# Performance work log

Hardware: AMD Instinct MI355X
Metric: run time of the kernel (lower is better)

## Reference

```python
import jax, jax.numpy as jnp
import numpy as np

DEPTH = 4  # truncation depth of the tensor algebra


def _tprod(a, b):
    # tensor (outer) product of level-i and level-j terms, flattened row-major
    # a: (B, C^i), b: (B, C^j) -> (B, C^(i+j))
    return (a[:, :, None] * b[:, None, :]).reshape(a.shape[0], -1)


def _exp_levels(dx):
    # exp(dx) in the truncated tensor algebra: level k = dx^{\otimes k} / k!
    levels = [dx]
    for k in range(2, DEPTH + 1):
        levels.append(_tprod(levels[-1], dx) / k)
    return tuple(levels)


def _chen(a, b):
    # Chen's identity: (a \otimes b)_k = a_k + b_k + sum_{i=1}^{k-1} a_i \otimes b_{k-i}
    out = []
    for k in range(1, DEPTH + 1):
        t = a[k - 1] + b[k - 1]
        for i in range(1, k):
            t = t + _tprod(a[i - 1], b[k - 1 - i])
        out.append(t)
    return tuple(out)


def _log_levels(s):
    # log(1 + x) = sum_{n>=1} (-1)^{n+1}/n x^{\otimes n}, x = S - 1 (levels 1..DEPTH)
    res = list(s)
    power = [t for t in s]  # x^{\otimes 1}; entries may become None (structurally zero)
    for n in range(2, DEPTH + 1):
        new = [None] * DEPTH
        for k in range(n, DEPTH + 1):
            acc = None
            for i in range(n - 1, k):
                if power[i - 1] is None:
                    continue
                term = _tprod(power[i - 1], s[k - i - 1])
                acc = term if acc is None else acc + term
            new[k - 1] = acc
        power = new
        coef = ((-1.0) ** (n + 1)) / n
        for k in range(n, DEPTH + 1):
            if power[k - 1] is not None:
                res[k - 1] = res[k - 1] + coef * power[k - 1]
    return tuple(res)


def _logsignature(path):
    # path: (B, L, C); no basepoint, stream=False, inverse=False, mode='expand'
    dxs = jnp.moveaxis(path[:, 1:] - path[:, :-1], 1, 0)  # (L-1, B, C)
    init = _exp_levels(dxs[0])

    def step(carry, dx):
        return _chen(carry, _exp_levels(dx)), None

    sig, _ = jax.lax.scan(step, init, dxs[1:])
    logsig = _log_levels(sig)
    return jnp.concatenate(logsig, axis=-1)  # (B, C + C^2 + ... + C^DEPTH)


def setup_inputs() -> dict:
    key = jax.random.key(0)
    # scale so high tensor-algebra levels stay well-conditioned in fp32
    path = 0.1 * jax.random.normal(key, (64, 256, 16), dtype=jnp.float32)
    return {"path": path}


def reference(path):
    return _logsignature(path)
```

## Files before the change

### kernel.cpp

```cpp
#include <hip/hip_runtime.h>


#define NC 16
#define NL 256
#define NB 64
#define NSTEP 255
#define OUTB 69904
#define SIG123 4368
#define OFF_L2 16
#define OFF_L3 272
#define OFF_L4 4368

__global__ void k_dx(const float* __restrict__ path, float* __restrict__ dx) {
    int idx = blockIdx.x * blockDim.x + threadIdx.x;
    const int total = NB * NSTEP * NC;
    if (idx >= total) return;
    int i = idx & (NC - 1);
    int t = (idx >> 4) % NSTEP;
    int j = idx / (NC * NSTEP);
    dx[idx] = path[((size_t)j * NL + t + 1) * NC + i] - path[((size_t)j * NL + t) * NC + i];
}

__global__ __launch_bounds__(256, 4) void k_scan(const float* __restrict__ dx,
                                                 float* __restrict__ out,
                                                 float* __restrict__ sig123) {
    const int bid = blockIdx.x;
    const int j = bid >> 4;
    const int a = bid & 15;
    const int tid = threadIdx.x;
    const int b = tid >> 4;
    const int c = tid & 15;

    float s4[16];
#pragma unroll
    for (int d = 0; d < 16; ++d) s4[d] = 0.f;
    float s3 = 0.f, s2ab = 0.f, s1a = 0.f;

    const float* dxj = dx + (size_t)j * NSTEP * NC;

    for (int t = 0; t < NSTEP; ++t) {
        const float* r = dxj + t * NC;
        const float4 q0 = *(const float4*)(r);
        const float4 q1 = *(const float4*)(r + 4);
        const float4 q2 = *(const float4*)(r + 8);
        const float4 q3 = *(const float4*)(r + 12);
        const float dxa = r[a];
        const float dxb = r[b];
        const float dxc = r[c];

        const float pre4 = fmaf(dxb, fmaf(1.f / 6.f, s1a, (1.f / 24.f) * dxa), 0.5f * s2ab);
        const float T = fmaf(dxc, pre4, s3);

        const float dv[16] = {q0.x, q0.y, q0.z, q0.w, q1.x, q1.y, q1.z, q1.w,
                              q2.x, q2.y, q2.z, q2.w, q3.x, q3.y, q3.z, q3.w};
#pragma unroll
        for (int d = 0; d < 16; ++d) s4[d] = fmaf(dv[d], T, s4[d]);

        const float U = fmaf(dxb, fmaf(0.5f, s1a, (1.f / 6.f) * dxa), s2ab);
        s3 = fmaf(dxc, U, s3);
        s2ab = fmaf(dxb, fmaf(0.5f, dxa, s1a), s2ab);
        s1a += dxa;
    }

    float* outj = out + (size_t)j * OUTB;
    float* o4 = outj + OFF_L4 + ((a * 16 + b) * 16 + c) * 16;
#pragma unroll
    for (int d = 0; d < 16; d += 4)
        *(float4*)(o4 + d) = make_float4(s4[d], s4[d + 1], s4[d + 2], s4[d + 3]);

    float* sg = sig123 + (size_t)j * SIG123;
    sg[OFF_L3 + (a * 16 + b) * 16 + c] = s3;
    if (c == 0) sg[OFF_L2 + a * 16 + b] = s2ab;
    if (tid == 0) sg[a] = s1a;
}

__global__ __launch_bounds__(256) void k_log(const float* __restrict__ sig123,
                                             float* __restrict__ out) {
    const int bid = blockIdx.x;
    const int j = bid >> 4;
    const int a = bid & 15;
    const int tid = threadIdx.x;
    const int b = tid >> 4;
    const int c = tid & 15;

    const float* sg = sig123 + (size_t)j * SIG123;
    const float* s1 = sg;
    const float* s2 = sg + OFF_L2;
    const float* s3 = sg + OFF_L3;

    const float s1a = s1[a], s1b = s1[b], s1c = s1[c];
    const float s2ab = s2[a * 16 + b];
    const float s2bc = s2[b * 16 + c];
    const float s3abc = s3[(a * 16 + b) * 16 + c];

    float* outj = out + (size_t)j * OUTB;

    const float A = -0.5f * s1a;
    const float Bv = fmaf((1.f / 3.f) * s1a, s1b, -0.5f * s2ab);
    const float Cv = -0.5f * s3abc + (1.f / 3.f) * fmaf(s1a, s2bc, s2ab * s1c)
                     - 0.25f * s1a * s1b * s1c;

    float* o4 = outj + OFF_L4 + ((a * 16 + b) * 16 + c) * 16;
    const float* s3v = s3 + (b * 16 + c) * 16;
    const float* s2v = s2 + c * 16;
#pragma unroll
    for (int d0 = 0; d0 < 16; d0 += 4) {
        float4 v4 = *(const float4*)(o4 + d0);
        float4 v3 = *(const float4*)(s3v + d0);
        float4 v2 = *(const float4*)(s2v + d0);
        float4 v1 = *(const float4*)(s1 + d0);
        float4 rr;
        rr.x = fmaf(A, v3.x, v4.x) + fmaf(Bv, v2.x, Cv * v1.x);
        rr.y = fmaf(A, v3.y, v4.y) + fmaf(Bv, v2.y, Cv * v1.y);
        rr.z = fmaf(A, v3.z, v4.z) + fmaf(Bv, v2.z, Cv * v1.z);
        rr.w = fmaf(A, v3.w, v4.w) + fmaf(Bv, v2.w, Cv * v1.w);
        *(float4*)(o4 + d0) = rr;
    }

    const float r3 = s3abc - 0.5f * fmaf(s1a, s2bc, s2ab * s1c)
                     + (1.f / 3.f) * s1a * s1b * s1c;
    outj[OFF_L3 + (a * 16 + b) * 16 + c] = r3;
    if (c == 0) outj[OFF_L2 + a * 16 + b] = fmaf(-0.5f * s1a, s1b, s2ab);
    if (tid == 0) outj[a] = s1a;
}

extern "C" void kernel_launch(void* const* d_in, const int* in_sizes, int n_in,
                              void* d_out, int out_size, void* d_ws, size_t ws_size,
                              hipStream_t stream) {
    const float* path = (const float*)d_in[0];
    float* out = (float*)d_out;
    float* dx = (float*)d_ws;
    float* sig123 = dx + (size_t)NB * NSTEP * NC;

    const int total_dx = NB * NSTEP * NC;
    k_dx<<<(total_dx + 255) / 256, 256, 0, stream>>>(path, dx);
    k_scan<<<NB * 16, 256, 0, stream>>>(dx, out, sig123);
    k_log<<<NB * 16, 256, 0, stream>>>(sig123, out);
}
```

Before: 130.4 us.

## Add transposed dx copy, vectorize scan scalar loads, coalesce level-4 stores via LDS

k_dx now stages each path in shared memory and writes two copies of the increments: the row-major layout and a transposed per-channel layout. k_scan reads its per-thread scalars dxa/dxb/dxc as float4 from the transposed copy, four steps at a time, so the scattered scalar loads are replaced with vector loads. The level-4 result is staged through LDS so each block writes a contiguous 16 KB region, and k_log is remapped to read and write that region contiguously. The cost is an extra workspace buffer, extra write traffic in k_dx, a k_dx grid of only NB blocks, and more index math in k_log.

New measurement: 124.8 us. 1.04x faster.

```diff
diff --git a/kernel.cpp b/kernel.cpp
--- a/kernel.cpp
+++ b/kernel.cpp
@@ -11,17 +11,38 @@
 #define OFF_L3 272
 #define OFF_L4 4368
 
-__global__ void k_dx(const float* __restrict__ path, float* __restrict__ dx) {
-    int idx = blockIdx.x * blockDim.x + threadIdx.x;
-    const int total = NB * NSTEP * NC;
-    if (idx >= total) return;
-    int i = idx & (NC - 1);
-    int t = (idx >> 4) % NSTEP;
-    int j = idx / (NC * NSTEP);
-    dx[idx] = path[((size_t)j * NL + t + 1) * NC + i] - path[((size_t)j * NL + t) * NC + i];
-}
-
-__global__ __launch_bounds__(256, 4) void k_scan(const float* __restrict__ dx,
+#define DX1_OFF 0
+#define DXT_OFF 261120
+#define SIG_OFF (261120 + 262144)
+
+__global__ __launch_bounds__(256) void k_dx(const float* __restrict__ path,
+                                            float* __restrict__ dx1,
+                                            float* __restrict__ dxt) {
+    const int j = blockIdx.x;
+    const int tid = threadIdx.x;
+    __shared__ float L[NL * NC];
+
+    const float* pj = path + (size_t)j * NL * NC;
+#pragma unroll
+    for (int k = 0; k < 4; ++k) {
+        const int f = tid + k * 256;
+        *(float4*)&L[f * 4] = *(const float4*)&pj[f * 4];
+    }
+    __syncthreads();
+
+    float* d1 = dx1 + (size_t)j * NSTEP * NC;
+    for (int f = tid; f < NSTEP * NC; f += 256) d1[f] = L[f + NC] - L[f];
+
+    float* dt = dxt + (size_t)j * NC * 256;
+#pragma unroll
+    for (int k = 0; k < NC; ++k) {
+        const int t = tid;
+        if (t < NSTEP) dt[k * 256 + t] = L[(t + 1) * NC + k] - L[t * NC + k];
+    }
+}
+
+__global__ __launch_bounds__(256, 4) void k_scan(const float* __restrict__ dx1,
+                                                 const float* __restrict__ dxt,
                                                  float* __restrict__ out,
                                                  float* __restrict__ sig123) {
     const int bid = blockIdx.x;
@@ -36,37 +57,73 @@
     for (int d = 0; d < 16; ++d) s4[d] = 0.f;
     float s3 = 0.f, s2ab = 0.f, s1a = 0.f;
 
-    const float* dxj = dx + (size_t)j * NSTEP * NC;
-
-    for (int t = 0; t < NSTEP; ++t) {
-        const float* r = dxj + t * NC;
+    const float* row0 = dx1 + (size_t)j * NSTEP * NC;
+    const float* ra = dxt + ((size_t)j * NC + a) * 256;
+    const float* rb = dxt + ((size_t)j * NC + b) * 256;
+    const float* rc = dxt + ((size_t)j * NC + c) * 256;
+
+    int t = 0;
+    for (int it = 0; it < 63; ++it, t += 4) {
+        const float4 vb = *(const float4*)(rb + t);
+        const float4 vc = *(const float4*)(rc + t);
+        const float4 va = *(const float4*)(ra + t);
+#pragma unroll
+        for (int u = 0; u < 4; ++u) {
+            const float* r = row0 + (t + u) * NC;
+            const float4 q0 = *(const float4*)(r);
+            const float4 q1 = *(const float4*)(r + 4);
+            const float4 q2 = *(const float4*)(r + 8);
+            const float4 q3 = *(const float4*)(r + 12);
+            const float dxa = (u == 0) ? va.x : (u == 1) ? va.y : (u == 2) ? va.z : va.w;
+            const float dxb = (u == 0) ? vb.x : (u == 1) ? vb.y : (u == 2) ? vb.z : vb.w;
+            const float dxc = (u == 0) ? vc.x : (u == 1) ? vc.y : (u == 2) ? vc.z : vc.w;
+
+            const float pre4 = fmaf(dxb, fmaf(1.f / 6.f, s1a, (1.f / 24.f) * dxa), 0.5f * s2ab);
+            const float T = fmaf(dxc, pre4, s3);
+            const float dv[16] = {q0.x, q0.y, q0.z, q0.w, q1.x, q1.y, q1.z, q1.w,
+                                  q2.x, q2.y, q2.z, q2.w, q3.x, q3.y, q3.z, q3.w};
+#pragma unroll
+            for (int d = 0; d < 16; ++d) s4[d] = fmaf(dv[d], T, s4[d]);
+
+            const float U = fmaf(dxb, fmaf(0.5f, s1a, (1.f / 6.f) * dxa), s2ab);
+            s3 = fmaf(dxc, U, s3);
+            s2ab = fmaf(dxb, fmaf(0.5f, dxa, s1a), s2ab);
+            s1a += dxa;
+        }
+    }
+    for (; t < NSTEP; ++t) {
+        const float* r = row0 + t * NC;
         const float4 q0 = *(const float4*)(r);
         const float4 q1 = *(const float4*)(r + 4);
         const float4 q2 = *(const float4*)(r + 8);
         const float4 q3 = *(const float4*)(r + 12);
-        const float dxa = r[a];
-        const float dxb = r[b];
-        const float dxc = r[c];
-
+        const float dxa = ra[t];
+        const float dxb = rb[t];
+        const float dxc = rc[t];
         const float pre4 = fmaf(dxb, fmaf(1.f / 6.f, s1a, (1.f / 24.f) * dxa), 0.5f * s2ab);
         const float T = fmaf(dxc, pre4, s3);
-
         const float dv[16] = {q0.x, q0.y, q0.z, q0.w, q1.x, q1.y, q1.z, q1.w,
                               q2.x, q2.y, q2.z, q2.w, q3.x, q3.y, q3.z, q3.w};
 #pragma unroll
         for (int d = 0; d < 16; ++d) s4[d] = fmaf(dv[d], T, s4[d]);
-
         const float U = fmaf(dxb, fmaf(0.5f, s1a, (1.f / 6.f) * dxa), s2ab);
         s3 = fmaf(dxc, U, s3);
         s2ab = fmaf(dxb, fmaf(0.5f, dxa, s1a), s2ab);
         s1a += dxa;
     }
 
-    float* outj = out + (size_t)j * OUTB;
-    float* o4 = outj + OFF_L4 + ((a * 16 + b) * 16 + c) * 16;
+    __shared__ float ls[4096];
 #pragma unroll
     for (int d = 0; d < 16; d += 4)
-        *(float4*)(o4 + d) = make_float4(s4[d], s4[d + 1], s4[d + 2], s4[d + 3]);
+        *(float4*)&ls[tid * 16 + d] = make_float4(s4[d], s4[d + 1], s4[d + 2], s4[d + 3]);
+    __syncthreads();
+
+    float* o4 = out + (size_t)j * OUTB + OFF_L4 + a * 4096;
+#pragma unroll
+    for (int k = 0; k < 4; ++k) {
+        const int f = tid + k * 256;
+        *(float4*)(o4 + f * 4) = *(const float4*)&ls[f * 4];
+    }
 
     float* sg = sig123 + (size_t)j * SIG123;
     sg[OFF_L3 + (a * 16 + b) * 16 + c] = s3;
@@ -80,47 +137,57 @@
     const int j = bid >> 4;
     const int a = bid & 15;
     const int tid = threadIdx.x;
-    const int b = tid >> 4;
-    const int c = tid & 15;
 
     const float* sg = sig123 + (size_t)j * SIG123;
     const float* s1 = sg;
     const float* s2 = sg + OFF_L2;
     const float* s3 = sg + OFF_L3;
 
-    const float s1a = s1[a], s1b = s1[b], s1c = s1[c];
-    const float s2ab = s2[a * 16 + b];
-    const float s2bc = s2[b * 16 + c];
-    const float s3abc = s3[(a * 16 + b) * 16 + c];
-
+    const float s1a = s1[a];
     float* outj = out + (size_t)j * OUTB;
-
+    float* o4 = outj + OFF_L4 + a * 4096;
     const float A = -0.5f * s1a;
-    const float Bv = fmaf((1.f / 3.f) * s1a, s1b, -0.5f * s2ab);
-    const float Cv = -0.5f * s3abc + (1.f / 3.f) * fmaf(s1a, s2bc, s2ab * s1c)
-                     - 0.25f * s1a * s1b * s1c;
-
-    float* o4 = outj + OFF_L4 + ((a * 16 + b) * 16 + c) * 16;
-    const float* s3v = s3 + (b * 16 + c) * 16;
-    const float* s2v = s2 + c * 16;
-#pragma unroll
-    for (int d0 = 0; d0 < 16; d0 += 4) {
-        float4 v4 = *(const float4*)(o4 + d0);
-        float4 v3 = *(const float4*)(s3v + d0);
-        float4 v2 = *(const float4*)(s2v + d0);
-        float4 v1 = *(const float4*)(s1 + d0);
+
+#pragma unroll
+    for (int k = 0; k < 4; ++k) {
+        const int f = tid + k * 256;
+        const int m0 = f * 4;
+        const int b = m0 >> 8;
+        const int c = (m0 >> 4) & 15;
+        const float s1b = s1[b], s1c = s1[c];
+        const float s2ab = s2[a * 16 + b];
+        const float s2bc = s2[b * 16 + c];
+        const float s3abc = s3[m0 >> 4];
+        const float s3abc_real = s3[(a * 16 + b) * 16 + c];
+        (void)s3abc;
+
+        const float Bv = fmaf((1.f / 3.f) * s1a, s1b, -0.5f * s2ab);
+        const float Cv = -0.5f * s3abc_real + (1.f / 3.f) * fmaf(s1a, s2bc, s2ab * s1c)
+                         - 0.25f * s1a * s1b * s1c;
+
+        const float4 v4 = *(const float4*)(o4 + m0);
+        const float4 v3 = *(const float4*)(s3 + m0);
+        const float4 v2 = *(const float4*)(s2 + (m0 & 255));
+        const float4 v1 = *(const float4*)(s1 + (m0 & 15));
         float4 rr;
         rr.x = fmaf(A, v3.x, v4.x) + fmaf(Bv, v2.x, Cv * v1.x);
         rr.y = fmaf(A, v3.y, v4.y) + fmaf(Bv, v2.y, Cv * v1.y);
         rr.z = fmaf(A, v3.z, v4.z) + fmaf(Bv, v2.z, Cv * v1.z);
         rr.w = fmaf(A, v3.w, v4.w) + fmaf(Bv, v2.w, Cv * v1.w);
-        *(float4*)(o4 + d0) = rr;
-    }
-
-    const float r3 = s3abc - 0.5f * fmaf(s1a, s2bc, s2ab * s1c)
-                     + (1.f / 3.f) * s1a * s1b * s1c;
-    outj[OFF_L3 + (a * 16 + b) * 16 + c] = r3;
-    if (c == 0) outj[OFF_L2 + a * 16 + b] = fmaf(-0.5f * s1a, s1b, s2ab);
+        *(float4*)(o4 + m0) = rr;
+    }
+
+    {
+        const int b = tid >> 4, c = tid & 15;
+        const float s1b = s1[b], s1c = s1[c];
+        const float s2ab = s2[a * 16 + b];
+        const float s2bc = s2[b * 16 + c];
+        const float s3abc = s3[(a * 16 + b) * 16 + c];
+        const float r3 = s3abc - 0.5f * fmaf(s1a, s2bc, s2ab * s1c)
+                         + (1.f / 3.f) * s1a * s1b * s1c;
+        outj[OFF_L3 + a * 256 + tid] = r3;
+    }
+    if (tid < 16) outj[OFF_L2 + a * 16 + tid] = fmaf(-0.5f * s1a, s1[tid], s2[a * 16 + tid]);
     if (tid == 0) outj[a] = s1a;
 }
 
@@ -129,11 +196,12 @@
                               hipStream_t stream) {
     const float* path = (const float*)d_in[0];
     float* out = (float*)d_out;
-    float* dx = (float*)d_ws;
-    float* sig123 = dx + (size_t)NB * NSTEP * NC;
-
-    const int total_dx = NB * NSTEP * NC;
-    k_dx<<<(total_dx + 255) / 256, 256, 0, stream>>>(path, dx);
-    k_scan<<<NB * 16, 256, 0, stream>>>(dx, out, sig123);
+    float* ws = (float*)d_ws;
+    float* dx1 = ws + DX1_OFF;
+    float* dxt = ws + DXT_OFF;
+    float* sig123 = ws + SIG_OFF;
+
+    k_dx<<<NB, 256, 0, stream>>>(path, dx1, dxt);
+    k_scan<<<NB * 16, 256, 0, stream>>>(dx1, dxt, out, sig123);
     k_log<<<NB * 16, 256, 0, stream>>>(sig123, out);
 }
```
